# Kernel tuning notes

Measured on AMD Instinct MI355X. Metric: run time of the kernel, lower is better.

Reference implementation:

```python
import jax, jax.numpy as jnp
import numpy as np

EMBED_DIM = 512
NUM_HEADS = 8
NUM_LAYERS = 2
LN_EPS = 1e-5


def setup_inputs() -> dict:
    key = jax.random.key(0)
    ks = jax.random.split(key, 12)
    B, S, E, L = 8, 1024, EMBED_DIM, NUM_LAYERS
    scale = 1.0 / np.sqrt(E)  # kaiming-ish init scale for 1x1 conv weights
    return {
        "x": jax.random.normal(ks[0], (B, S, E), jnp.float32),
        "adj": jax.random.uniform(ks[1], (S, S), jnp.float32),
        "Wq": jax.random.normal(ks[2], (L, E, E), jnp.float32) * scale,
        "bq": jnp.zeros((L, E), jnp.float32),
        "Wk": jax.random.normal(ks[3], (L, E, E), jnp.float32) * scale,
        "bk": jnp.zeros((L, E), jnp.float32),
        "Wv": jax.random.normal(ks[4], (L, E, E), jnp.float32) * scale,
        "bv": jnp.zeros((L, E), jnp.float32),
        "Wo": jax.random.normal(ks[5], (L, E, E), jnp.float32) * scale,
        "bo": jnp.zeros((L, E), jnp.float32),
        "gamma": jnp.ones((L, E), jnp.float32),
        "beta": jnp.zeros((L, E), jnp.float32),
    }


def _layer_norm(x, g, b):
    mu = jnp.mean(x, axis=-1, keepdims=True)
    var = jnp.mean(jnp.square(x - mu), axis=-1, keepdims=True)
    return (x - mu) * jax.lax.rsqrt(var + LN_EPS) * g + b


def reference(x, adj, Wq, bq, Wk, bk, Wv, bv, Wo, bo, gamma, beta):
    B, S, E = x.shape
    H = NUM_HEADS
    D = E // H
    inv_sqrt_d = 1.0 / np.sqrt(D)
    for l in range(Wq.shape[0]):
        # 1x1 Conv2d over channel dim == per-token linear: out_f = sum_e W[f,e] x_e + b_f
        q = (jnp.einsum('bse,fe->bsf', x, Wq[l]) + bq[l]).reshape(B, S, H, D).transpose(0, 2, 1, 3)
        k = (jnp.einsum('bse,fe->bsf', x, Wk[l]) + bk[l]).reshape(B, S, H, D).transpose(0, 2, 1, 3)
        v = (jnp.einsum('bse,fe->bsf', x, Wv[l]) + bv[l]).reshape(B, S, H, D).transpose(0, 2, 1, 3)
        # adjacency-gated scaled dot-product attention: multiplicative mask BEFORE softmax
        scores = jnp.einsum('bhqd,bhkd->bhqk', q, k) * inv_sqrt_d
        scores = scores * adj  # broadcast [S,S] over [B,H,S,S]
        attn = jax.nn.softmax(scores, axis=-1)
        out = jnp.einsum('bhqk,bhkd->bhqd', attn, v)
        out = out.transpose(0, 2, 1, 3).reshape(B, S, E)
        out = jnp.einsum('bse,fe->bsf', out, Wo[l]) + bo[l]
        x = _layer_norm(x + out, gamma[l], beta[l])
    return x
```

## Files before the change

kernel.cpp:

```cpp
#include <hip/hip_runtime.h>
#include <stdint.h>

typedef _Float16 f16;
typedef _Float16 f16x8 __attribute__((ext_vector_type(8)));
typedef _Float16 f16x4 __attribute__((ext_vector_type(4)));
typedef float f32x4 __attribute__((ext_vector_type(4)));

constexpr int EMB = 512;
constexpr int SEQ = 1024;
constexpr int NH = 8;
constexpr int DHEAD = 64;
constexpr int NTOK = 8192;

#define GAS __attribute__((address_space(1)))
#define LAS __attribute__((address_space(3)))

#if __has_builtin(__builtin_amdgcn_exp2f)
#define EXP2F(x) __builtin_amdgcn_exp2f(x)
#else
#define EXP2F(x) exp2f(x)
#endif

#define SCHED_BAR() __builtin_amdgcn_sched_barrier(0)

static __device__ __forceinline__ void gload_lds16(const void* g, void* l) {
  __builtin_amdgcn_global_load_lds((const GAS void*)g, (LAS void*)l, 16, 0, 0);
}


__global__ void k_pack_w(const float* __restrict__ Wq, const float* __restrict__ Wk,
                         const float* __restrict__ Wv, const float* __restrict__ Wo,
                         f16* __restrict__ wqkv, f16* __restrict__ wo) {
  int tid = blockIdx.x * 256 + threadIdx.x;
  if (tid < 2 * 1536 * 128) {
    int e4 = tid & 127;
    int f = (tid >> 7) % 1536;
    int l = tid / (128 * 1536);
    int part = f >> 9, fr = f & 511;
    const float* src = (part == 0 ? Wq : part == 1 ? Wk : Wv) + (size_t)l * EMB * EMB + (size_t)fr * EMB + e4 * 4;
    float4 v = *(const float4*)src;
    f16x4 hv = {(f16)v.x, (f16)v.y, (f16)v.z, (f16)v.w};
    *(f16x4*)(wqkv + ((size_t)l * 1536 + f) * EMB + e4 * 4) = hv;
  }
  if (tid < 2 * 512 * 128) {
    int e4 = tid & 127;
    int f = (tid >> 7) % 512;
    int l = tid / (128 * 512);
    float4 v = *(const float4*)(Wo + (size_t)l * EMB * EMB + (size_t)f * EMB + e4 * 4);
    f16x4 hv = {(f16)v.x, (f16)v.y, (f16)v.z, (f16)v.w};
    *(f16x4*)(wo + ((size_t)l * 512 + f) * EMB + e4 * 4) = hv;
  }
}

__global__ void k_pack_b(const float* __restrict__ bq, const float* __restrict__ bk,
                         const float* __restrict__ bv, float* __restrict__ bqkv) {
  int tid = blockIdx.x * 256 + threadIdx.x;
  if (tid < 2 * 1536) {
    int f = tid % 1536, l = tid / 1536;
    int part = f >> 9, fr = f & 511;
    bqkv[tid] = (part == 0 ? bq : part == 1 ? bk : bv)[l * EMB + fr];
  }
}

__global__ void k_cvt(const float* __restrict__ x, f16* __restrict__ out) {
  int i = (blockIdx.x * 256 + threadIdx.x) * 8;
  float4 a = *(const float4*)(x + i);
  float4 b = *(const float4*)(x + i + 4);
  f16x8 h = {(f16)a.x, (f16)a.y, (f16)a.z, (f16)a.w, (f16)b.x, (f16)b.y, (f16)b.z, (f16)b.w};
  *(f16x8*)(out + i) = h;
}

__global__ void k_pack_adjP(const float* __restrict__ adj, f16* __restrict__ adjP) {
  int tid = blockIdx.x * 256 + threadIdx.x;
  int lo = tid & 15, t = (tid >> 4) & 15, qrow = tid >> 8;
  const float c = 0.125f * 1.44269504088896f;
  const float* row = adj + (size_t)qrow * SEQ + t * 64 + lo;
  f16x4 v = {(f16)(row[0] * c), (f16)(row[16] * c), (f16)(row[32] * c), (f16)(row[48] * c)};
  *(f16x4*)(adjP + (size_t)tid * 4) = v;
}


template <int MODE, int BK>
__global__ __launch_bounds__(256) void k_gemm(const f16* __restrict__ A, const f16* __restrict__ Bw,
                                              const float* __restrict__ bias, f16* __restrict__ Uout,
                                              f16* __restrict__ Qo, f16* __restrict__ Ko,
                                              f16* __restrict__ Vt) {
  constexpr int CH = 128 * BK / 8;
  constexpr int NT = EMB / BK;
  __shared__ f16x8 sA[3][CH];
  __shared__ f16x8 sB[3][CH];
  const int tid = threadIdx.x;
  const int lane = tid & 63;
  const int lanelow = lane & 15, lanehi = lane >> 4;
  const int wave = tid >> 6;
  const int wm = wave >> 1, wn = wave & 1;
  const int flat = blockIdx.x;
  const int mt = (flat & 7) * 8 + ((flat >> 3) & 7);
  const int nt = flat >> 6;
  const int m0 = mt * 128, n0 = nt * 128;

  f32x4 acc[4][4] = {};

  const f16* aB = A + (size_t)m0 * EMB;
  const f16* bB = Bw + (size_t)n0 * EMB;

  int srow[4], scl[4];
#pragma unroll
  for (int p = 0; p < (BK == 64 ? 4 : 2); ++p) {
    int c = p * 256 + tid;
    if (BK == 64) {
      srow[p] = c >> 3;
      scl[p] = (c & 7) ^ (srow[p] & 7);
    } else {
      int R = c >> 3, sub = c & 7;
      srow[p] = R * 2 + (sub >> 2);
      scl[p] = (sub & 3) ^ (R & 3);
    }
  }

#define GSTAGE(ktv, bufv)                                                                     \
  {                                                                                           \
    _Pragma("unroll") for (int p = 0; p < (BK == 64 ? 4 : 2); ++p) {                          \
      int c = p * 256 + tid;                                                                  \
      gload_lds16(aB + (size_t)srow[p] * EMB + (ktv) + scl[p] * 8, (char*)sA[bufv] + c * 16); \
      gload_lds16(bB + (size_t)srow[p] * EMB + (ktv) + scl[p] * 8, (char*)sB[bufv] + c * 16); \
    }                                                                                         \
  }

  GSTAGE(0, 0);
  GSTAGE(BK, 1);

  int cur = 0;
  for (int t = 0; t < NT; ++t) {
    SCHED_BAR();
    if (t < NT - 1) {
      if (BK == 64) asm volatile("s_waitcnt vmcnt(8)");
      else          asm volatile("s_waitcnt vmcnt(4)");
    } else {
      asm volatile("s_waitcnt vmcnt(0)");
    }
    SCHED_BAR();
    __builtin_amdgcn_s_barrier();
    SCHED_BAR();
    if (t < NT - 2) GSTAGE((t + 2) * BK, (cur == 0) ? 2 : cur - 1);

    const f16x8* sAc = sA[cur];
    const f16x8* sBc = sB[cur];
#pragma unroll
    for (int ks = 0; ks < BK / 32; ++ks) {
      f16x8 af[4], bf[4];
#pragma unroll
      for (int m = 0; m < 4; ++m) {
        int r = wm * 64 + m * 16 + lanelow;
        af[m] = (BK == 64) ? sAc[r * 8 + ((ks * 4 + lanehi) ^ (r & 7))]
                           : sAc[(r >> 1) * 8 + (r & 1) * 4 + (lanehi ^ ((r >> 1) & 3))];
      }
#pragma unroll
      for (int n = 0; n < 4; ++n) {
        int r = wn * 64 + n * 16 + lanelow;
        bf[n] = (BK == 64) ? sBc[r * 8 + ((ks * 4 + lanehi) ^ (r & 7))]
                           : sBc[(r >> 1) * 8 + (r & 1) * 4 + (lanehi ^ ((r >> 1) & 3))];
      }
      __builtin_amdgcn_s_setprio(1);
#pragma unroll
      for (int m = 0; m < 4; ++m)
#pragma unroll
        for (int n = 0; n < 4; ++n)
          acc[m][n] = __builtin_amdgcn_mfma_f32_16x16x32_f16(af[m], bf[n], acc[m][n], 0, 0, 0);
      __builtin_amdgcn_s_setprio(0);
    }
    cur = (cur == 2) ? 0 : cur + 1;
  }
#undef GSTAGE

#pragma unroll
  for (int n = 0; n < 4; ++n) {
    int col = n0 + wn * 64 + n * 16 + lanelow;
    float bv = bias[col];
    if (MODE == 1 && (col >> 9) == 2) {
      int fr = col & 511, hh = fr >> 6, d = fr & 63;
#pragma unroll
      for (int m = 0; m < 4; ++m) {
        int rbase = m0 + wm * 64 + m * 16 + lanehi * 4;
        int b = rbase >> 10, s = rbase & 1023;
        f16x4 pv = {(f16)(acc[m][n][0] + bv), (f16)(acc[m][n][1] + bv),
                    (f16)(acc[m][n][2] + bv), (f16)(acc[m][n][3] + bv)};
        *(f16x4*)(Vt + ((size_t)(b * NH + hh) * DHEAD + d) * SEQ + s) = pv;
      }
    } else {
#pragma unroll
      for (int m = 0; m < 4; ++m) {
        int rbase = m0 + wm * 64 + m * 16 + lanehi * 4;
#pragma unroll
        for (int j = 0; j < 4; ++j) {
          float v = acc[m][n][j] + bv;
          int row = rbase + j;
          if (MODE == 0) {
            Uout[(size_t)row * EMB + col] = (f16)v;
          } else {
            int part = col >> 9, fr = col & 511;
            int hh = fr >> 6, d = fr & 63;
            int b = row >> 10, s = row & 1023;
            int bh = b * NH + hh;
            if (part == 0)
              Qo[((size_t)bh * SEQ + s) * DHEAD + d] = (f16)v;
            else
              Ko[((size_t)bh * SEQ + s) * DHEAD + d] = (f16)v;
          }
        }
      }
    }
  }
}


__global__ __launch_bounds__(512) void k_attn(const f16* __restrict__ Q, const f16* __restrict__ K,
                                              const f16* __restrict__ Vt, const f16* __restrict__ adjP,
                                              f16* __restrict__ Ob) {
  __shared__ __align__(16) f16 sK[2][8192];
  __shared__ __align__(16) f16 sV[2][8192];
  __shared__ __align__(16) f16 Pl[8 * 1024];
  const int tid = threadIdx.x;
  const int lane = tid & 63;
  const int lanelow = lane & 15, lanehi = lane >> 4;
  const int wave = tid >> 6;
  f16* Plw = Pl + wave * 1024;

  const int flat = blockIdx.x;
  const int bh = (flat & 7) * 8 + ((flat >> 3) & 7);
  const int qblk = flat >> 6;
  const int b = bh >> 3, hh = bh & 7;
  const int q0 = qblk * 128 + wave * 16;

  const f16* Kbase = K + (size_t)bh * SEQ * DHEAD;
  const f16* Vbase = Vt + (size_t)bh * DHEAD * SEQ;

  int kr[2], kc[2], vr[2], vc[2];
#pragma unroll
  for (int p = 0; p < 2; ++p) {
    int c = p * 512 + tid;
    kr[p] = c >> 3;
    kc[p] = (c & 7) ^ (kr[p] & 7);
    vr[p] = c >> 4;
    vc[p] = (c & 15) ^ (vr[p] & 7);
  }

#define STAGE(tv, bufv)                                                                         \
  {                                                                                             \
    const int kts = (tv)*128;                                                                   \
    _Pragma("unroll") for (int p = 0; p < 2; ++p) {                                             \
      int c = p * 512 + tid;                                                                    \
      gload_lds16(Kbase + (size_t)(kts + kr[p]) * DHEAD + kc[p] * 8, (char*)sK[bufv] + c * 16); \
      gload_lds16(Vbase + (size_t)vr[p] * SEQ + kts + vc[p] * 8, (char*)sV[bufv] + c * 16);     \
    }                                                                                           \
  }

  f16x8 qf[2];
#pragma unroll
  for (int ks = 0; ks < 2; ++ks)
    qf[ks] = *(const f16x8*)(Q + ((size_t)bh * SEQ + q0 + lanelow) * DHEAD + ks * 32 + lanehi * 8);

  const f16* Ab = adjP + ((size_t)(q0 + lanehi * 4) * 256 + lanelow) * 4;
  f16x4 ab[4];
#define LOAD_A(tv)                                                           \
  {                                                                          \
    _Pragma("unroll") for (int j = 0; j < 4; ++j)                            \
        ab[j] = *(const f16x4*)(Ab + ((size_t)j * 256 + (tv)*16) * 4);       \
  }

  f32x4 oacc[4] = {};
  float lpart[4] = {};

  STAGE(0, 0);
  LOAD_A(0);
  __syncthreads();

  int cur = 0;
  for (int t = 0; t < 8; ++t) {
    if (t < 7) STAGE(t + 1, cur ^ 1);

    const f16* sKc = sK[cur];
    const f16* sVc = sV[cur];

#pragma unroll
    for (int hs = 0; hs < 2; ++hs) {
      const int t2 = t * 2 + hs;

      f32x4 sacc[4] = {};
#pragma unroll
      for (int ks = 0; ks < 2; ++ks) {
        f16x8 kf[4];
#pragma unroll
        for (int n = 0; n < 4; ++n) {
          int r = hs * 64 + n * 16 + lanelow;
          kf[n] = *(const f16x8*)(sKc + (r * 8 + ((ks * 4 + lanehi) ^ (r & 7))) * 8);
        }
        __builtin_amdgcn_s_setprio(1);
#pragma unroll
        for (int n = 0; n < 4; ++n)
          sacc[n] = __builtin_amdgcn_mfma_f32_16x16x32_f16(qf[ks], kf[n], sacc[n], 0, 0, 0);
        __builtin_amdgcn_s_setprio(0);
      }

      f16x4 acur[4];
#pragma unroll
      for (int j = 0; j < 4; ++j) acur[j] = ab[j];
      if (t2 < 15) LOAD_A(t2 + 1);

#pragma unroll
      for (int nh = 0; nh < 2; ++nh) {
#pragma unroll
        for (int j = 0; j < 4; ++j) {
          const int prow = lanehi * 4 + j;
          const f16x4 a4 = acur[j];
#pragma unroll
          for (int nn = 0; nn < 2; ++nn) {
            const int n = nh * 2 + nn;
            float p = EXP2F(sacc[n][j] * (float)a4[n]);
            lpart[j] += p;
            Plw[prow * 64 + (((n * 2 + (lanelow >> 3)) ^ (prow & 7)) * 8) + (lanelow & 7)] = (f16)p;
          }
        }
        f16x8 pa, vf[4];
        pa = *(const f16x8*)(Plw + lanelow * 64 + (((nh * 4 + lanehi) ^ (lanelow & 7)) * 8));
#pragma unroll
        for (int n = 0; n < 4; ++n) {
          int r = n * 16 + lanelow;
          vf[n] = *(const f16x8*)(sVc + (r * 16 + ((hs * 8 + nh * 4 + lanehi) ^ (r & 7))) * 8);
        }
        __builtin_amdgcn_s_setprio(1);
#pragma unroll
        for (int n = 0; n < 4; ++n)
          oacc[n] = __builtin_amdgcn_mfma_f32_16x16x32_f16(pa, vf[n], oacc[n], 0, 0, 0);
        __builtin_amdgcn_s_setprio(0);
      }
    }

    __syncthreads();
    cur ^= 1;
  }
#undef STAGE
#undef LOAD_A

  float linv[4];
#pragma unroll
  for (int j = 0; j < 4; ++j) {
    float l = lpart[j];
#pragma unroll
    for (int off = 1; off < 16; off <<= 1) l += __shfl_xor(l, off, 16);
    linv[j] = 1.0f / l;
  }
#pragma unroll
  for (int n = 0; n < 4; ++n)
#pragma unroll
    for (int j = 0; j < 4; ++j) {
      int qrow = q0 + lanehi * 4 + j;
      float v = oacc[n][j] * linv[j];
      Ob[((size_t)b * SEQ + qrow) * EMB + hh * DHEAD + n * 16 + lanelow] = (f16)v;
    }
}


template <int INH>
__global__ __launch_bounds__(256) void k_ln(const float* __restrict__ xf, const f16* __restrict__ xh_in,
                                            const f16* __restrict__ Uin,
                                            const float* __restrict__ gamma, const float* __restrict__ beta,
                                            float* __restrict__ xout, f16* __restrict__ xh_out) {
  const int row = blockIdx.x * 4 + (threadIdx.x >> 6);
  const int lane = threadIdx.x & 63;
  const size_t base = (size_t)row * EMB + lane * 8;
  float u[8];
  {
    f16x8 uh = *(const f16x8*)(Uin + base);
    if (INH) {
      f16x8 xh8 = *(const f16x8*)(xh_in + base);
#pragma unroll
      for (int i = 0; i < 8; ++i) u[i] = (float)xh8[i] + (float)uh[i];
    } else {
      float4 a0 = *(const float4*)(xf + base);
      float4 a1 = *(const float4*)(xf + base + 4);
      u[0] = a0.x + (float)uh[0]; u[1] = a0.y + (float)uh[1];
      u[2] = a0.z + (float)uh[2]; u[3] = a0.w + (float)uh[3];
      u[4] = a1.x + (float)uh[4]; u[5] = a1.y + (float)uh[5];
      u[6] = a1.z + (float)uh[6]; u[7] = a1.w + (float)uh[7];
    }
  }
  float s = 0.f;
#pragma unroll
  for (int i = 0; i < 8; ++i) s += u[i];
#pragma unroll
  for (int off = 1; off < 64; off <<= 1) s += __shfl_xor(s, off, 64);
  const float mu = s * (1.0f / EMB);
  float v = 0.f;
#pragma unroll
  for (int i = 0; i < 8; ++i) { float d = u[i] - mu; v += d * d; }
#pragma unroll
  for (int off = 1; off < 64; off <<= 1) v += __shfl_xor(v, off, 64);
  const float rs = rsqrtf(v * (1.0f / EMB) + 1e-5f);
  const int ci = lane * 8;
  float4 g0 = *(const float4*)(gamma + ci);
  float4 g1 = *(const float4*)(gamma + ci + 4);
  float4 b0 = *(const float4*)(beta + ci);
  float4 b1 = *(const float4*)(beta + ci + 4);
  float g[8] = {g0.x, g0.y, g0.z, g0.w, g1.x, g1.y, g1.z, g1.w};
  float be[8] = {b0.x, b0.y, b0.z, b0.w, b1.x, b1.y, b1.z, b1.w};
  float o[8];
#pragma unroll
  for (int i = 0; i < 8; ++i) o[i] = (u[i] - mu) * rs * g[i] + be[i];
  if (xout) {
    float4 o0 = {o[0], o[1], o[2], o[3]}, o1 = {o[4], o[5], o[6], o[7]};
    *(float4*)(xout + base) = o0;
    *(float4*)(xout + base + 4) = o1;
  }
  if (xh_out) {
    f16x8 hv = {(f16)o[0], (f16)o[1], (f16)o[2], (f16)o[3], (f16)o[4], (f16)o[5], (f16)o[6], (f16)o[7]};
    *(f16x8*)(xh_out + base) = hv;
  }
}


extern "C" void kernel_launch(void* const* d_in, const int* in_sizes, int n_in,
                              void* d_out, int out_size, void* d_ws, size_t ws_size,
                              hipStream_t stream) {
  (void)in_sizes; (void)n_in; (void)out_size; (void)ws_size;
  const float* x = (const float*)d_in[0];
  const float* adj = (const float*)d_in[1];
  const float* Wq = (const float*)d_in[2];
  const float* bq = (const float*)d_in[3];
  const float* Wk = (const float*)d_in[4];
  const float* bk = (const float*)d_in[5];
  const float* Wv = (const float*)d_in[6];
  const float* bv = (const float*)d_in[7];
  const float* Wo = (const float*)d_in[8];
  const float* bo = (const float*)d_in[9];
  const float* gamma = (const float*)d_in[10];
  const float* beta = (const float*)d_in[11];

  char* ws = (char*)d_ws;
  size_t off = 0;
  auto alloc = [&](size_t bytes) {
    char* p = ws + off;
    off += (bytes + 255) & ~(size_t)255;
    return p;
  };
  f16* wqkv = (f16*)alloc((size_t)2 * 1536 * 512 * sizeof(f16));
  f16* wo = (f16*)alloc((size_t)2 * 512 * 512 * sizeof(f16));
  float* bqkv = (float*)alloc((size_t)2 * 1536 * sizeof(float));
  f16* adjP = (f16*)alloc((size_t)SEQ * SEQ * sizeof(f16));
  f16* xh = (f16*)alloc((size_t)NTOK * EMB * sizeof(f16));
  f16* Qb = (f16*)alloc((size_t)NTOK * EMB * sizeof(f16));
  f16* Kb = (f16*)alloc((size_t)NTOK * EMB * sizeof(f16));
  f16* Vtb = (f16*)alloc((size_t)NTOK * EMB * sizeof(f16));
  f16* Ob = (f16*)alloc((size_t)NTOK * EMB * sizeof(f16));
  f16* U = (f16*)alloc((size_t)NTOK * EMB * sizeof(f16));

  k_pack_w<<<1536, 256, 0, stream>>>(Wq, Wk, Wv, Wo, wqkv, wo);
  k_pack_b<<<12, 256, 0, stream>>>(bq, bk, bv, bqkv);
  k_pack_adjP<<<1024, 256, 0, stream>>>(adj, adjP);
  k_cvt<<<2048, 256, 0, stream>>>(x, xh);

  for (int l = 0; l < 2; ++l) {
    k_gemm<1, 32><<<768, 256, 0, stream>>>(xh, wqkv + (size_t)l * 1536 * 512, bqkv + l * 1536,
                                           nullptr, Qb, Kb, Vtb);
    k_attn<<<512, 512, 0, stream>>>(Qb, Kb, Vtb, adjP, Ob);
    k_gemm<0, 64><<<256, 256, 0, stream>>>(Ob, wo + (size_t)l * 512 * 512, bo + l * 512,
                                           U, nullptr, nullptr, nullptr);
    if (l == 0)
      k_ln<0><<<2048, 256, 0, stream>>>(x, nullptr, U, gamma, beta, nullptr, xh);
    else
      k_ln<1><<<2048, 256, 0, stream>>>(nullptr, xh, U, gamma + 512, beta + 512, (float*)d_out, nullptr);
  }
}
```

Before: 163.6 us.

## Restructure projection GEMM to 8 waves with double-buffered LDS

The projection GEMM moves from 256 threads with 64x64 per-wave tiles and a 3-stage hand-synchronised prefetch to 512 threads with 32x64 per-wave tiles. The pipeline becomes a 2-buffer scheme guarded by __syncthreads, and BK is fixed at 64 for both the QKV and output GEMMs. The intent is more waves per block to hide latency and simpler synchronisation. In exchange each wave reuses fewer loaded fragments, each wave does more LDS reads per MFMA, and the prefetch depth is shallower than before.

```diff
diff --git a/kernel.cpp b/kernel.cpp
--- a/kernel.cpp
+++ b/kernel.cpp
@@ -20,8 +20,6 @@
 #else
 #define EXP2F(x) exp2f(x)
 #endif
-
-#define SCHED_BAR() __builtin_amdgcn_sched_barrier(0)
 
 static __device__ __forceinline__ void gload_lds16(const void* g, void* l) {
   __builtin_amdgcn_global_load_lds((const GAS void*)g, (LAS void*)l, 16, 0, 0);
@@ -80,96 +78,75 @@
 }
 
 
-template <int MODE, int BK>
-__global__ __launch_bounds__(256) void k_gemm(const f16* __restrict__ A, const f16* __restrict__ Bw,
+template <int MODE>
+__global__ __launch_bounds__(512) void k_gemm(const f16* __restrict__ A, const f16* __restrict__ Bw,
                                               const float* __restrict__ bias, f16* __restrict__ Uout,
                                               f16* __restrict__ Qo, f16* __restrict__ Ko,
                                               f16* __restrict__ Vt) {
-  constexpr int CH = 128 * BK / 8;
-  constexpr int NT = EMB / BK;
-  __shared__ f16x8 sA[3][CH];
-  __shared__ f16x8 sB[3][CH];
+  __shared__ f16x8 sA[2][1024];
+  __shared__ f16x8 sB[2][1024];
   const int tid = threadIdx.x;
   const int lane = tid & 63;
   const int lanelow = lane & 15, lanehi = lane >> 4;
   const int wave = tid >> 6;
-  const int wm = wave >> 1, wn = wave & 1;
+  const int wm = wave >> 1;
+  const int wn = wave & 1;
   const int flat = blockIdx.x;
   const int mt = (flat & 7) * 8 + ((flat >> 3) & 7);
   const int nt = flat >> 6;
   const int m0 = mt * 128, n0 = nt * 128;
 
-  f32x4 acc[4][4] = {};
+  f32x4 acc[2][4] = {};
 
   const f16* aB = A + (size_t)m0 * EMB;
   const f16* bB = Bw + (size_t)n0 * EMB;
 
-  int srow[4], scl[4];
-#pragma unroll
-  for (int p = 0; p < (BK == 64 ? 4 : 2); ++p) {
-    int c = p * 256 + tid;
-    if (BK == 64) {
-      srow[p] = c >> 3;
-      scl[p] = (c & 7) ^ (srow[p] & 7);
-    } else {
-      int R = c >> 3, sub = c & 7;
-      srow[p] = R * 2 + (sub >> 2);
-      scl[p] = (sub & 3) ^ (R & 3);
-    }
+  int srow[2], scl[2];
+#pragma unroll
+  for (int p = 0; p < 2; ++p) {
+    int c = p * 512 + tid;
+    srow[p] = c >> 3;
+    scl[p] = (c & 7) ^ (srow[p] & 7);
   }
 
 #define GSTAGE(ktv, bufv)                                                                     \
   {                                                                                           \
-    _Pragma("unroll") for (int p = 0; p < (BK == 64 ? 4 : 2); ++p) {                          \
-      int c = p * 256 + tid;                                                                  \
+    _Pragma("unroll") for (int p = 0; p < 2; ++p) {                                           \
+      int c = p * 512 + tid;                                                                  \
       gload_lds16(aB + (size_t)srow[p] * EMB + (ktv) + scl[p] * 8, (char*)sA[bufv] + c * 16); \
       gload_lds16(bB + (size_t)srow[p] * EMB + (ktv) + scl[p] * 8, (char*)sB[bufv] + c * 16); \
     }                                                                                         \
   }
 
   GSTAGE(0, 0);
-  GSTAGE(BK, 1);
+  __syncthreads();
 
   int cur = 0;
-  for (int t = 0; t < NT; ++t) {
-    SCHED_BAR();
-    if (t < NT - 1) {
-      if (BK == 64) asm volatile("s_waitcnt vmcnt(8)");
-      else          asm volatile("s_waitcnt vmcnt(4)");
-    } else {
-      asm volatile("s_waitcnt vmcnt(0)");
-    }
-    SCHED_BAR();
-    __builtin_amdgcn_s_barrier();
-    SCHED_BAR();
-    if (t < NT - 2) GSTAGE((t + 2) * BK, (cur == 0) ? 2 : cur - 1);
-
-    const f16x8* sAc = sA[cur];
-    const f16x8* sBc = sB[cur];
-#pragma unroll
-    for (int ks = 0; ks < BK / 32; ++ks) {
-      f16x8 af[4], bf[4];
-#pragma unroll
-      for (int m = 0; m < 4; ++m) {
-        int r = wm * 64 + m * 16 + lanelow;
-        af[m] = (BK == 64) ? sAc[r * 8 + ((ks * 4 + lanehi) ^ (r & 7))]
-                           : sAc[(r >> 1) * 8 + (r & 1) * 4 + (lanehi ^ ((r >> 1) & 3))];
+  for (int t = 0; t < 8; ++t) {
+    if (t < 7) GSTAGE((t + 1) * 64, cur ^ 1);
+#pragma unroll
+    for (int ks = 0; ks < 2; ++ks) {
+      f16x8 af[2], bf[4];
+#pragma unroll
+      for (int m = 0; m < 2; ++m) {
+        int r = wm * 32 + m * 16 + lanelow;
+        af[m] = sA[cur][r * 8 + ((ks * 4 + lanehi) ^ (r & 7))];
       }
 #pragma unroll
       for (int n = 0; n < 4; ++n) {
         int r = wn * 64 + n * 16 + lanelow;
-        bf[n] = (BK == 64) ? sBc[r * 8 + ((ks * 4 + lanehi) ^ (r & 7))]
-                           : sBc[(r >> 1) * 8 + (r & 1) * 4 + (lanehi ^ ((r >> 1) & 3))];
+        bf[n] = sB[cur][r * 8 + ((ks * 4 + lanehi) ^ (r & 7))];
       }
       __builtin_amdgcn_s_setprio(1);
 #pragma unroll
-      for (int m = 0; m < 4; ++m)
+      for (int m = 0; m < 2; ++m)
 #pragma unroll
         for (int n = 0; n < 4; ++n)
           acc[m][n] = __builtin_amdgcn_mfma_f32_16x16x32_f16(af[m], bf[n], acc[m][n], 0, 0, 0);
       __builtin_amdgcn_s_setprio(0);
     }
-    cur = (cur == 2) ? 0 : cur + 1;
+    __syncthreads();
+    cur ^= 1;
   }
 #undef GSTAGE
 
@@ -180,8 +157,8 @@
     if (MODE == 1 && (col >> 9) == 2) {
       int fr = col & 511, hh = fr >> 6, d = fr & 63;
 #pragma unroll
-      for (int m = 0; m < 4; ++m) {
-        int rbase = m0 + wm * 64 + m * 16 + lanehi * 4;
+      for (int m = 0; m < 2; ++m) {
+        int rbase = m0 + wm * 32 + m * 16 + lanehi * 4;
         int b = rbase >> 10, s = rbase & 1023;
         f16x4 pv = {(f16)(acc[m][n][0] + bv), (f16)(acc[m][n][1] + bv),
                     (f16)(acc[m][n][2] + bv), (f16)(acc[m][n][3] + bv)};
@@ -189,8 +166,8 @@
       }
     } else {
 #pragma unroll
-      for (int m = 0; m < 4; ++m) {
-        int rbase = m0 + wm * 64 + m * 16 + lanehi * 4;
+      for (int m = 0; m < 2; ++m) {
+        int rbase = m0 + wm * 32 + m * 16 + lanehi * 4;
 #pragma unroll
         for (int j = 0; j < 4; ++j) {
           float v = acc[m][n][j] + bv;
@@ -460,11 +437,11 @@
   k_cvt<<<2048, 256, 0, stream>>>(x, xh);
 
   for (int l = 0; l < 2; ++l) {
-    k_gemm<1, 32><<<768, 256, 0, stream>>>(xh, wqkv + (size_t)l * 1536 * 512, bqkv + l * 1536,
-                                           nullptr, Qb, Kb, Vtb);
+    k_gemm<1><<<768, 512, 0, stream>>>(xh, wqkv + (size_t)l * 1536 * 512, bqkv + l * 1536,
+                                       nullptr, Qb, Kb, Vtb);
     k_attn<<<512, 512, 0, stream>>>(Qb, Kb, Vtb, adjP, Ob);
-    k_gemm<0, 64><<<256, 256, 0, stream>>>(Ob, wo + (size_t)l * 512 * 512, bo + l * 512,
-                                           U, nullptr, nullptr, nullptr);
+    k_gemm<0><<<256, 512, 0, stream>>>(Ob, wo + (size_t)l * 512 * 512, bo + l * 512,
+                                       U, nullptr, nullptr, nullptr);
     if (l == 0)
       k_ln<0><<<2048, 256, 0, stream>>>(x, nullptr, U, gamma, beta, nullptr, xh);
     else
```

After: 163.9 us. About the same (+0.2%).
